# Kernel tuning notes

Hardware: AMD Instinct MI355X
Metric: run time of the kernel (lower is better)

Reference implementation:

```python
import jax, jax.numpy as jnp
import numpy as np

N = [80000, 70000, 50000]   # entities per type (flattened over the ragged batch)
F = [64, 128, 48]           # feature width per entity type
D = 512                     # d_model
B = 64                      # number of episodes in the ragged batch
EPS_IN = 1e-4               # InputNorm eps
EPS_LN = 1e-5               # LayerNorm eps
CLIP = 5.0                  # InputNorm cliprange


def setup_inputs() -> dict:
    key = jax.random.key(0)
    ks = jax.random.split(key, 3 * 7 + 2)
    inp = {}
    for i, (n, f) in enumerate(zip(N, F)):
        base = 7 * i
        inp[f"ent{i}"] = jax.random.normal(ks[base], (n, f), dtype=jnp.float32)
        inp[f"mean{i}"] = 0.1 * jax.random.normal(ks[base + 1], (f,), dtype=jnp.float32)
        inp[f"var{i}"] = jax.random.uniform(ks[base + 2], (f,), minval=0.5, maxval=1.5, dtype=jnp.float32)
        inp[f"W{i}"] = jax.random.normal(ks[base + 3], (f, D), dtype=jnp.float32) / np.sqrt(f)
        inp[f"b{i}"] = jnp.zeros((D,), dtype=jnp.float32)
        inp[f"gamma{i}"] = jnp.ones((D,), dtype=jnp.float32)
        inp[f"beta{i}"] = jnp.zeros((D,), dtype=jnp.float32)
    total = sum(N)
    # index_map: permutation reassembling per-type blocks into ragged episode order
    inp["index_map"] = jax.random.permutation(ks[-2], total).astype(jnp.int64)
    inp["batch_index"] = jnp.sort(jax.random.randint(ks[-1], (total,), 0, B)).astype(jnp.int64)
    return inp


def _embed(x, mean, var, W, b, gamma, beta):
    # InputNorm: normalize with running stats, clip outliers
    h = jnp.clip((x - mean) * jax.lax.rsqrt(var + EPS_IN), -CLIP, CLIP)
    # Linear + ReLU
    h = jnp.maximum(h @ W + b, 0.0)
    # LayerNorm
    mu = h.mean(-1, keepdims=True)
    v = ((h - mu) ** 2).mean(-1, keepdims=True)
    return gamma * (h - mu) * jax.lax.rsqrt(v + EPS_LN) + beta


def reference(ent0, mean0, var0, W0, b0, gamma0, beta0,
              ent1, mean1, var1, W1, b1, gamma1, beta1,
              ent2, mean2, var2, W2, b2, gamma2, beta2,
              index_map, batch_index):
    embeds = [
        _embed(ent0, mean0, var0, W0, b0, gamma0, beta0),
        _embed(ent1, mean1, var1, W1, b1, gamma1, beta1),
        _embed(ent2, mean2, var2, W2, b2, gamma2, beta2),
    ]
    x = jnp.concatenate(embeds, axis=0)                      # [sum(N), D]
    entity_type = jnp.concatenate(
        [jnp.full((n, 1), float(i), dtype=jnp.float32) for i, n in enumerate(N)], axis=0
    )
    # ragged reorder: gather-based reassembly into episode-major order
    x = x[index_map]
    entity_types = entity_type[index_map]
    tbatch_index = batch_index[index_map]
    return x, tbatch_index, entity_types
```

## Files before the change

kernel.cpp:

```cpp
#include <hip/hip_runtime.h>

#define DMODEL 512
#define EPS_IN 1e-4f
#define EPS_LN 1e-5f
#define CLIPV  5.0f

typedef float f32x4 __attribute__((ext_vector_type(4)));
typedef short s16x8 __attribute__((ext_vector_type(8)));

__device__ __forceinline__ unsigned short f2bf(float f) {
    union { float f; unsigned u; } v; v.f = f;
    unsigned r = v.u + 0x7fffu + ((v.u >> 16) & 1u);
    return (unsigned short)(r >> 16);
}

struct TypeParams {
    const float* x; const float* mean; const float* var;
    const unsigned short* Wt;
    const float* b; const float* gamma; const float* beta;
    int n;
    int offset;
    int nb;
};

__global__ __launch_bounds__(256) void setup_kernel(
    const int* __restrict__ index_map, const int* __restrict__ batch_index,
    int* __restrict__ inv, float* __restrict__ out_t, float* __restrict__ out_e,
    int total, int n0, int n01)
{
    const int j = blockIdx.x * 256 + threadIdx.x;
    if (j >= total) return;
    const int r = index_map[j];
    inv[r] = j;
    out_t[j] = (float)batch_index[r];
    out_e[j] = (r < n0) ? 0.0f : ((r < n01) ? 1.0f : 2.0f);
}

__global__ __launch_bounds__(256) void prep_w(
    const float* __restrict__ W0, const float* __restrict__ W1, const float* __restrict__ W2,
    unsigned short* __restrict__ Wt0, unsigned short* __restrict__ Wt1, unsigned short* __restrict__ Wt2)
{
    int idx = blockIdx.x * 256 + threadIdx.x;
    const float* W; unsigned short* Wt; int K, Kp;
    if (idx < DMODEL * 64)              { W = W0; Wt = Wt0; K = 64;  Kp = 64; }
    else if (idx < DMODEL * (64 + 128)) { idx -= DMODEL * 64;  W = W1; Wt = Wt1; K = 128; Kp = 128; }
    else if (idx < DMODEL * 256)        { idx -= DMODEL * 192; W = W2; Wt = Wt2; K = 48;  Kp = 64; }
    else return;
    const int nn = idx / Kp, k = idx - nn * Kp;
    const float w = (k < K) ? W[(size_t)k * DMODEL + nn] : 0.0f;
    Wt[idx] = f2bf(w);
}

template<int F, int KP>
__device__ __forceinline__ void embed_body(
    const TypeParams& p, int bid, const int* __restrict__ inv,
    float* __restrict__ out, char* lds)
{
    const int tid  = threadIdx.x;
    const int lane = tid & 63;
    const int w    = tid >> 6;
    const int wm   = w >> 2;
    const int wn   = w & 3;
    const int l15  = lane & 15;
    const int g    = lane >> 4;
    const int row0 = bid * 64;
    const int n    = p.n;

    constexpr int SEG = KP / 8;
    for (int idx = tid; idx < 64 * SEG; idx += 512) {
        const int r = idx / SEG;
        const int s = idx - r * SEG;
        const int c = s * 8;
        const int gr = row0 + r;
        s16x8 pk;
        if (gr < n && c < F) {
            const float4 x0 = *(const float4*)(p.x + (size_t)gr * F + c);
            const float4 x1 = *(const float4*)(p.x + (size_t)gr * F + c + 4);
            const float4 m0 = *(const float4*)(p.mean + c);
            const float4 m1 = *(const float4*)(p.mean + c + 4);
            const float4 v0 = *(const float4*)(p.var + c);
            const float4 v1 = *(const float4*)(p.var + c + 4);
            float t[8] = {x0.x - m0.x, x0.y - m0.y, x0.z - m0.z, x0.w - m0.w,
                          x1.x - m1.x, x1.y - m1.y, x1.z - m1.z, x1.w - m1.w};
            const float iv[8] = {rsqrtf(v0.x + EPS_IN), rsqrtf(v0.y + EPS_IN),
                                 rsqrtf(v0.z + EPS_IN), rsqrtf(v0.w + EPS_IN),
                                 rsqrtf(v1.x + EPS_IN), rsqrtf(v1.y + EPS_IN),
                                 rsqrtf(v1.z + EPS_IN), rsqrtf(v1.w + EPS_IN)};
#pragma unroll
            for (int jj = 0; jj < 8; ++jj)
                pk[jj] = (short)f2bf(fminf(fmaxf(t[jj] * iv[jj], -CLIPV), CLIPV));
        } else {
#pragma unroll
            for (int jj = 0; jj < 8; ++jj) pk[jj] = 0;
        }
        int byte = r * (KP * 2) + s * 16;
        byte ^= (r & 7) << 4;
        *reinterpret_cast<s16x8*>(lds + byte) = pk;
    }
    __syncthreads();

    f32x4 acc[2][8];
#pragma unroll
    for (int m = 0; m < 2; ++m)
#pragma unroll
        for (int t = 0; t < 8; ++t) acc[m][t] = (f32x4)0.0f;

    const int arow = wm * 32 + l15;
    const unsigned short* wtl = p.Wt + (size_t)(wn * 128 + l15) * KP + g * 8;

#pragma unroll
    for (int ks = 0; ks < KP / 32; ++ks) {
        const int kb = ks * 64 + g * 16;
        int a0b = arow * (KP * 2) + kb;        a0b ^= (arow & 7) << 4;
        int a1b = (arow + 16) * (KP * 2) + kb; a1b ^= (arow & 7) << 4;
        const s16x8 a0 = *reinterpret_cast<const s16x8*>(lds + a0b);
        const s16x8 a1 = *reinterpret_cast<const s16x8*>(lds + a1b);
#pragma unroll
        for (int t = 0; t < 8; ++t) {
            const s16x8 bf = *reinterpret_cast<const s16x8*>(wtl + (size_t)t * 16 * KP + ks * 32);
            acc[0][t] = __builtin_amdgcn_mfma_f32_16x16x32_bf16(a0, bf, acc[0][t], 0, 0, 0);
            acc[1][t] = __builtin_amdgcn_mfma_f32_16x16x32_bf16(a1, bf, acc[1][t], 0, 0, 0);
        }
    }

    float bv[8], gv[8], ev[8];
#pragma unroll
    for (int t = 0; t < 8; ++t) {
        const int col = wn * 128 + t * 16 + l15;
        bv[t] = p.b[col]; gv[t] = p.gamma[col]; ev[t] = p.beta[col];
    }

    float ps[2][4] = {{0}}, pq[2][4] = {{0}};
#pragma unroll
    for (int m = 0; m < 2; ++m)
#pragma unroll
        for (int t = 0; t < 8; ++t)
#pragma unroll
            for (int j = 0; j < 4; ++j) {
                const float v = fmaxf(acc[m][t][j] + bv[t], 0.0f);
                ps[m][j] += v;
                pq[m][j] = fmaf(v, v, pq[m][j]);
            }
#pragma unroll
    for (int off = 1; off < 16; off <<= 1)
#pragma unroll
        for (int m = 0; m < 2; ++m)
#pragma unroll
            for (int j = 0; j < 4; ++j) {
                ps[m][j] += __shfl_xor(ps[m][j], off, 64);
                pq[m][j] += __shfl_xor(pq[m][j], off, 64);
            }

    float2* red = reinterpret_cast<float2*>(lds + 64 * KP * 2);
    if (l15 == 0) {
#pragma unroll
        for (int m = 0; m < 2; ++m)
#pragma unroll
            for (int j = 0; j < 4; ++j) {
                const int rl = wm * 32 + m * 16 + 4 * g + j;
                red[rl * 4 + wn] = make_float2(ps[m][j], pq[m][j]);
            }
    }
    __syncthreads();

    float mu[2][4], sc[2][4]; int orow[2][4]; bool okr[2][4];
#pragma unroll
    for (int m = 0; m < 2; ++m)
#pragma unroll
        for (int j = 0; j < 4; ++j) {
            const int rl = wm * 32 + m * 16 + 4 * g + j;
            float s = 0.0f, q = 0.0f;
#pragma unroll
            for (int wq = 0; wq < 4; ++wq) { const float2 e = red[rl * 4 + wq]; s += e.x; q += e.y; }
            const float mmu = s * (1.0f / DMODEL);
            const float vv  = fmaxf(q * (1.0f / DMODEL) - mmu * mmu, 0.0f);
            mu[m][j] = mmu;
            sc[m][j] = rsqrtf(vv + EPS_LN);
            const int rg = row0 + rl;
            okr[m][j] = (rg < n);
            orow[m][j] = okr[m][j] ? inv[p.offset + rg] : 0;
        }

#pragma unroll
    for (int m = 0; m < 2; ++m)
#pragma unroll
        for (int j = 0; j < 4; ++j) {
            if (!okr[m][j]) continue;
            float* op = out + (size_t)orow[m][j] * DMODEL + wn * 128 + l15;
            const float mmu = mu[m][j], ssc = sc[m][j];
#pragma unroll
            for (int t = 0; t < 8; ++t) {
                const float v = fmaxf(acc[m][t][j] + bv[t], 0.0f);
                op[t * 16] = fmaf(gv[t] * ssc, v - mmu, ev[t]);
            }
        }
}

__global__ __launch_bounds__(512) void embed_all(
    TypeParams p0, TypeParams p1, TypeParams p2,
    const int* __restrict__ inv, float* __restrict__ out)
{
    extern __shared__ char lds[];
    const int bid = blockIdx.x;
    if (bid < p0.nb)                embed_body<64, 64>  (p0, bid, inv, out, lds);
    else if (bid < p0.nb + p1.nb)   embed_body<128, 128>(p1, bid - p0.nb, inv, out, lds);
    else                            embed_body<48, 64>  (p2, bid - p0.nb - p1.nb, inv, out, lds);
}

extern "C" void kernel_launch(void* const* d_in, const int* in_sizes, int n_in,
                              void* d_out, int out_size, void* d_ws, size_t ws_size,
                              hipStream_t stream)
{
    const int F0 = 64, F1 = 128, F2 = 48;
    const int n0 = in_sizes[0]  / F0;
    const int n1 = in_sizes[7]  / F1;
    const int n2 = in_sizes[14] / F2;
    const int total = n0 + n1 + n2;

    float* out   = (float*)d_out;
    float* out_t = out + (size_t)total * DMODEL;
    float* out_e = out_t + total;

    int* inv = (int*)d_ws;
    unsigned short* Wt0 = (unsigned short*)((char*)d_ws + ((size_t)total * 4 + 255 & ~(size_t)255));
    unsigned short* Wt1 = Wt0 + DMODEL * 64;
    unsigned short* Wt2 = Wt1 + DMODEL * 128;

    const int* index_map   = (const int*)d_in[21];
    const int* batch_index = (const int*)d_in[22];

    setup_kernel<<<(total + 255) / 256, 256, 0, stream>>>(
        index_map, batch_index, inv, out_t, out_e, total, n0, n0 + n1);

    prep_w<<<(DMODEL * 256 + 255) / 256, 256, 0, stream>>>(
        (const float*)d_in[3], (const float*)d_in[10], (const float*)d_in[17],
        Wt0, Wt1, Wt2);

    TypeParams p0{(const float*)d_in[0],  (const float*)d_in[1],  (const float*)d_in[2],
                  Wt0, (const float*)d_in[4],  (const float*)d_in[5],  (const float*)d_in[6],
                  n0, 0,       (n0 + 63) / 64};
    TypeParams p1{(const float*)d_in[7],  (const float*)d_in[8],  (const float*)d_in[9],
                  Wt1, (const float*)d_in[11], (const float*)d_in[12], (const float*)d_in[13],
                  n1, n0,      (n1 + 63) / 64};
    TypeParams p2{(const float*)d_in[14], (const float*)d_in[15], (const float*)d_in[16],
                  Wt2, (const float*)d_in[18], (const float*)d_in[19], (const float*)d_in[20],
                  n2, n0 + n1, (n2 + 63) / 64};

    const int nb = p0.nb + p1.nb + p2.nb;
    const int lds_size = 64 * 128 * 2 + 64 * 4 * sizeof(float2);
    embed_all<<<nb, 512, lds_size, stream>>>(p0, p1, p2, inv, out);
}
```

Baseline: 191.7 us.

## Halve embed tile to 32 rows with 4 waves, merge setup kernels

Shrinks each embed block from 64 rows/8 waves to 32 rows/4 waves, so every wave covers all 32 rows and a 128-column slice. Launch bounds become (256,4) to raise occupancy, and LDS per block is halved. The index-setup and weight-prep kernels are merged into one launch to save a kernel launch. The trade-off is twice as many blocks, each rereading the weight tile, and more per-block overhead.

```diff
diff --git a/kernel.cpp b/kernel.cpp
--- a/kernel.cpp
+++ b/kernel.cpp
@@ -23,32 +23,31 @@
     int nb;
 };
 
-__global__ __launch_bounds__(256) void setup_kernel(
+__global__ __launch_bounds__(256) void setup_all(
     const int* __restrict__ index_map, const int* __restrict__ batch_index,
     int* __restrict__ inv, float* __restrict__ out_t, float* __restrict__ out_e,
-    int total, int n0, int n01)
-{
-    const int j = blockIdx.x * 256 + threadIdx.x;
-    if (j >= total) return;
-    const int r = index_map[j];
-    inv[r] = j;
-    out_t[j] = (float)batch_index[r];
-    out_e[j] = (r < n0) ? 0.0f : ((r < n01) ? 1.0f : 2.0f);
-}
-
-__global__ __launch_bounds__(256) void prep_w(
+    int total, int n0, int n01, int nbA,
     const float* __restrict__ W0, const float* __restrict__ W1, const float* __restrict__ W2,
     unsigned short* __restrict__ Wt0, unsigned short* __restrict__ Wt1, unsigned short* __restrict__ Wt2)
 {
-    int idx = blockIdx.x * 256 + threadIdx.x;
-    const float* W; unsigned short* Wt; int K, Kp;
-    if (idx < DMODEL * 64)              { W = W0; Wt = Wt0; K = 64;  Kp = 64; }
-    else if (idx < DMODEL * (64 + 128)) { idx -= DMODEL * 64;  W = W1; Wt = Wt1; K = 128; Kp = 128; }
-    else if (idx < DMODEL * 256)        { idx -= DMODEL * 192; W = W2; Wt = Wt2; K = 48;  Kp = 64; }
-    else return;
-    const int nn = idx / Kp, k = idx - nn * Kp;
-    const float w = (k < K) ? W[(size_t)k * DMODEL + nn] : 0.0f;
-    Wt[idx] = f2bf(w);
+    if (blockIdx.x < (unsigned)nbA) {
+        const int j = blockIdx.x * 256 + threadIdx.x;
+        if (j >= total) return;
+        const int r = index_map[j];
+        inv[r] = j;
+        out_t[j] = (float)batch_index[r];
+        out_e[j] = (r < n0) ? 0.0f : ((r < n01) ? 1.0f : 2.0f);
+    } else {
+        int idx = (blockIdx.x - nbA) * 256 + threadIdx.x;
+        const float* W; unsigned short* Wt; int K, Kp;
+        if (idx < DMODEL * 64)              { W = W0; Wt = Wt0; K = 64;  Kp = 64; }
+        else if (idx < DMODEL * (64 + 128)) { idx -= DMODEL * 64;  W = W1; Wt = Wt1; K = 128; Kp = 128; }
+        else if (idx < DMODEL * 256)        { idx -= DMODEL * 192; W = W2; Wt = Wt2; K = 48;  Kp = 64; }
+        else return;
+        const int nn = idx / Kp, k = idx - nn * Kp;
+        const float w = (k < K) ? W[(size_t)k * DMODEL + nn] : 0.0f;
+        Wt[idx] = f2bf(w);
+    }
 }
 
 template<int F, int KP>
@@ -58,16 +57,15 @@
 {
     const int tid  = threadIdx.x;
     const int lane = tid & 63;
-    const int w    = tid >> 6;
-    const int wm   = w >> 2;
-    const int wn   = w & 3;
+    const int wn   = tid >> 6;
     const int l15  = lane & 15;
     const int g    = lane >> 4;
-    const int row0 = bid * 64;
+    const int row0 = bid * 32;
     const int n    = p.n;
 
     constexpr int SEG = KP / 8;
-    for (int idx = tid; idx < 64 * SEG; idx += 512) {
+#pragma unroll
+    for (int idx = tid; idx < 32 * SEG; idx += 256) {
         const int r = idx / SEG;
         const int s = idx - r * SEG;
         const int c = s * 8;
@@ -80,8 +78,8 @@
             const float4 m1 = *(const float4*)(p.mean + c + 4);
             const float4 v0 = *(const float4*)(p.var + c);
             const float4 v1 = *(const float4*)(p.var + c + 4);
-            float t[8] = {x0.x - m0.x, x0.y - m0.y, x0.z - m0.z, x0.w - m0.w,
-                          x1.x - m1.x, x1.y - m1.y, x1.z - m1.z, x1.w - m1.w};
+            const float t[8] = {x0.x - m0.x, x0.y - m0.y, x0.z - m0.z, x0.w - m0.w,
+                                x1.x - m1.x, x1.y - m1.y, x1.z - m1.z, x1.w - m1.w};
             const float iv[8] = {rsqrtf(v0.x + EPS_IN), rsqrtf(v0.y + EPS_IN),
                                  rsqrtf(v0.z + EPS_IN), rsqrtf(v0.w + EPS_IN),
                                  rsqrtf(v1.x + EPS_IN), rsqrtf(v1.y + EPS_IN),
@@ -105,14 +103,13 @@
 #pragma unroll
         for (int t = 0; t < 8; ++t) acc[m][t] = (f32x4)0.0f;
 
-    const int arow = wm * 32 + l15;
     const unsigned short* wtl = p.Wt + (size_t)(wn * 128 + l15) * KP + g * 8;
 
 #pragma unroll
     for (int ks = 0; ks < KP / 32; ++ks) {
         const int kb = ks * 64 + g * 16;
-        int a0b = arow * (KP * 2) + kb;        a0b ^= (arow & 7) << 4;
-        int a1b = (arow + 16) * (KP * 2) + kb; a1b ^= (arow & 7) << 4;
+        int a0b = l15 * (KP * 2) + kb;        a0b ^= (l15 & 7) << 4;
+        int a1b = (l15 + 16) * (KP * 2) + kb; a1b ^= (l15 & 7) << 4;
         const s16x8 a0 = *reinterpret_cast<const s16x8*>(lds + a0b);
         const s16x8 a1 = *reinterpret_cast<const s16x8*>(lds + a1b);
 #pragma unroll
@@ -130,73 +127,67 @@
         bv[t] = p.b[col]; gv[t] = p.gamma[col]; ev[t] = p.beta[col];
     }
 
-    float ps[2][4] = {{0}}, pq[2][4] = {{0}};
+    {
+        float ps[2][4] = {{0}}, pq[2][4] = {{0}};
+#pragma unroll
+        for (int m = 0; m < 2; ++m)
+#pragma unroll
+            for (int t = 0; t < 8; ++t)
+#pragma unroll
+                for (int j = 0; j < 4; ++j) {
+                    const float v = fmaxf(acc[m][t][j] + bv[t], 0.0f);
+                    ps[m][j] += v;
+                    pq[m][j] = fmaf(v, v, pq[m][j]);
+                }
+#pragma unroll
+        for (int off = 1; off < 16; off <<= 1)
+#pragma unroll
+            for (int m = 0; m < 2; ++m)
+#pragma unroll
+                for (int j = 0; j < 4; ++j) {
+                    ps[m][j] += __shfl_xor(ps[m][j], off, 64);
+                    pq[m][j] += __shfl_xor(pq[m][j], off, 64);
+                }
+
+        float2* red = reinterpret_cast<float2*>(lds + 32 * KP * 2);
+        if (l15 == 0) {
+#pragma unroll
+            for (int m = 0; m < 2; ++m)
+#pragma unroll
+                for (int j = 0; j < 4; ++j) {
+                    const int rl = m * 16 + 4 * g + j;
+                    red[rl * 4 + wn] = make_float2(ps[m][j], pq[m][j]);
+                }
+        }
+    }
+    __syncthreads();
+
+    const float2* red = reinterpret_cast<const float2*>(lds + 32 * KP * 2);
+
 #pragma unroll
     for (int m = 0; m < 2; ++m)
 #pragma unroll
-        for (int t = 0; t < 8; ++t)
-#pragma unroll
-            for (int j = 0; j < 4; ++j) {
-                const float v = fmaxf(acc[m][t][j] + bv[t], 0.0f);
-                ps[m][j] += v;
-                pq[m][j] = fmaf(v, v, pq[m][j]);
-            }
-#pragma unroll
-    for (int off = 1; off < 16; off <<= 1)
-#pragma unroll
-        for (int m = 0; m < 2; ++m)
-#pragma unroll
-            for (int j = 0; j < 4; ++j) {
-                ps[m][j] += __shfl_xor(ps[m][j], off, 64);
-                pq[m][j] += __shfl_xor(pq[m][j], off, 64);
-            }
-
-    float2* red = reinterpret_cast<float2*>(lds + 64 * KP * 2);
-    if (l15 == 0) {
-#pragma unroll
-        for (int m = 0; m < 2; ++m)
-#pragma unroll
-            for (int j = 0; j < 4; ++j) {
-                const int rl = wm * 32 + m * 16 + 4 * g + j;
-                red[rl * 4 + wn] = make_float2(ps[m][j], pq[m][j]);
-            }
-    }
-    __syncthreads();
-
-    float mu[2][4], sc[2][4]; int orow[2][4]; bool okr[2][4];
-#pragma unroll
-    for (int m = 0; m < 2; ++m)
-#pragma unroll
         for (int j = 0; j < 4; ++j) {
-            const int rl = wm * 32 + m * 16 + 4 * g + j;
+            const int rl = m * 16 + 4 * g + j;
+            const int rg = row0 + rl;
+            if (rg >= n) continue;
             float s = 0.0f, q = 0.0f;
 #pragma unroll
             for (int wq = 0; wq < 4; ++wq) { const float2 e = red[rl * 4 + wq]; s += e.x; q += e.y; }
-            const float mmu = s * (1.0f / DMODEL);
-            const float vv  = fmaxf(q * (1.0f / DMODEL) - mmu * mmu, 0.0f);
-            mu[m][j] = mmu;
-            sc[m][j] = rsqrtf(vv + EPS_LN);
-            const int rg = row0 + rl;
-            okr[m][j] = (rg < n);
-            orow[m][j] = okr[m][j] ? inv[p.offset + rg] : 0;
-        }
-
-#pragma unroll
-    for (int m = 0; m < 2; ++m)
-#pragma unroll
-        for (int j = 0; j < 4; ++j) {
-            if (!okr[m][j]) continue;
-            float* op = out + (size_t)orow[m][j] * DMODEL + wn * 128 + l15;
-            const float mmu = mu[m][j], ssc = sc[m][j];
+            const float mu = s * (1.0f / DMODEL);
+            const float vv = fmaxf(q * (1.0f / DMODEL) - mu * mu, 0.0f);
+            const float sc = rsqrtf(vv + EPS_LN);
+            const int orow = inv[p.offset + rg];
+            float* op = out + (size_t)orow * DMODEL + wn * 128 + l15;
 #pragma unroll
             for (int t = 0; t < 8; ++t) {
                 const float v = fmaxf(acc[m][t][j] + bv[t], 0.0f);
-                op[t * 16] = fmaf(gv[t] * ssc, v - mmu, ev[t]);
+                op[t * 16] = fmaf(gv[t] * sc, v - mu, ev[t]);
             }
         }
 }
 
-__global__ __launch_bounds__(512) void embed_all(
+__global__ __launch_bounds__(256, 4) void embed_all(
     TypeParams p0, TypeParams p1, TypeParams p2,
     const int* __restrict__ inv, float* __restrict__ out)
 {
@@ -222,31 +213,31 @@
     float* out_e = out_t + total;
 
     int* inv = (int*)d_ws;
-    unsigned short* Wt0 = (unsigned short*)((char*)d_ws + ((size_t)total * 4 + 255 & ~(size_t)255));
+    unsigned short* Wt0 = (unsigned short*)((char*)d_ws + (((size_t)total * 4 + 255) & ~(size_t)255));
     unsigned short* Wt1 = Wt0 + DMODEL * 64;
     unsigned short* Wt2 = Wt1 + DMODEL * 128;
 
     const int* index_map   = (const int*)d_in[21];
     const int* batch_index = (const int*)d_in[22];
 
-    setup_kernel<<<(total + 255) / 256, 256, 0, stream>>>(
-        index_map, batch_index, inv, out_t, out_e, total, n0, n0 + n1);
-
-    prep_w<<<(DMODEL * 256 + 255) / 256, 256, 0, stream>>>(
+    const int nbA = (total + 255) / 256;
+    const int nbB = (DMODEL * 256 + 255) / 256;
+    setup_all<<<nbA + nbB, 256, 0, stream>>>(
+        index_map, batch_index, inv, out_t, out_e, total, n0, n0 + n1, nbA,
         (const float*)d_in[3], (const float*)d_in[10], (const float*)d_in[17],
         Wt0, Wt1, Wt2);
 
     TypeParams p0{(const float*)d_in[0],  (const float*)d_in[1],  (const float*)d_in[2],
                   Wt0, (const float*)d_in[4],  (const float*)d_in[5],  (const float*)d_in[6],
-                  n0, 0,       (n0 + 63) / 64};
+                  n0, 0,       (n0 + 31) / 32};
     TypeParams p1{(const float*)d_in[7],  (const float*)d_in[8],  (const float*)d_in[9],
                   Wt1, (const float*)d_in[11], (const float*)d_in[12], (const float*)d_in[13],
-                  n1, n0,      (n1 + 63) / 64};
+                  n1, n0,      (n1 + 31) / 32};
     TypeParams p2{(const float*)d_in[14], (const float*)d_in[15], (const float*)d_in[16],
                   Wt2, (const float*)d_in[18], (const float*)d_in[19], (const float*)d_in[20],
-                  n2, n0 + n1, (n2 + 63) / 64};
+                  n2, n0 + n1, (n2 + 31) / 32};
 
     const int nb = p0.nb + p1.nb + p2.nb;
-    const int lds_size = 64 * 128 * 2 + 64 * 4 * sizeof(float2);
-    embed_all<<<nb, 512, lds_size, stream>>>(p0, p1, p2, inv, out);
-}
+    const int lds_size = 32 * 128 * 2 + 32 * 4 * sizeof(float2);
+    embed_all<<<nb, 256, lds_size, stream>>>(p0, p1, p2, inv, out);
+}
```

Result: faster. 162.1 us (-15.4%).
